# Optimization experiments

Measured on AMD Instinct MI355X. Metric: run time of the kernel, lower is better.

The kernel has to match this reference:

```python
import jax, jax.numpy as jnp
import numpy as np

# dims
N = 50000      # total nodes in merged batch graph
M = 250000     # edges for GNN propagation
E = 200000     # candidate edges scored by mixture-Bernoulli head
MAXN = 512     # max_num_nodes (padded adjacency row length)
H = 128        # hidden_dim = embedding_dim = msg_dim
EF = 128       # edge_feat_dim = 2 * att_edge_dim
ATT = 128      # att_hidden_dim
K = 20         # num_mix_component
L = 3          # num_GNN_layers
S = 512        # num_subgraph
B = 16         # batch of graphs
C = 1          # num_canonical_order


def setup_inputs() -> dict:
    key = jax.random.key(0)
    ks = list(jax.random.split(key, 64))
    it = iter(ks)
    nk = lambda: next(it)
    d = {}
    d['node_feat'] = jax.random.normal(nk(), (N, MAXN), jnp.float32)
    d['edge'] = jax.random.randint(nk(), (M, 2), 0, N, dtype=jnp.int32)
    d['edge_feat'] = jax.random.normal(nk(), (M, EF), jnp.float32)
    d['node_idx_gnn'] = jax.random.randint(nk(), (E, 2), 0, N, dtype=jnp.int32)
    d['label'] = (jax.random.uniform(nk(), (E,)) < 0.1).astype(jnp.float32)
    # even sorted partition of E candidate edges into S subgraphs (all nonempty)
    d['subgraph_idx'] = ((jnp.arange(E) * S) // E).astype(jnp.int32)
    # bc_idx = repeat_interleave(arange(B*C), subgraphs_per_graph)
    d['bc_idx'] = jnp.repeat(jnp.arange(B * C, dtype=jnp.int32), S // (B * C))
    # params
    def lin(k, out_d, in_d):
        return jax.random.normal(k, (out_d, in_d), jnp.float32) * (1.0 / np.sqrt(in_d))
    d['dec_W'] = lin(nk(), H, MAXN); d['dec_b'] = jnp.zeros((H,), jnp.float32)
    d['msg_W1'] = jnp.stack([lin(nk(), H, H + EF) for _ in range(L)])
    d['msg_b1'] = jnp.zeros((L, H), jnp.float32)
    d['msg_W2'] = jnp.stack([lin(nk(), H, H) for _ in range(L)])
    d['msg_b2'] = jnp.zeros((L, H), jnp.float32)
    d['att_W1'] = jnp.stack([lin(nk(), ATT, H + EF) for _ in range(L)])
    d['att_b1'] = jnp.zeros((L, ATT), jnp.float32)
    d['att_W2'] = jnp.stack([lin(nk(), H, ATT) for _ in range(L)])
    d['att_b2'] = jnp.zeros((L, H), jnp.float32)
    d['gru_Wih'] = jnp.stack([lin(nk(), 3 * H, H) for _ in range(L)])
    d['gru_bih'] = jnp.zeros((L, 3 * H), jnp.float32)
    d['gru_Whh'] = jnp.stack([lin(nk(), 3 * H, H) for _ in range(L)])
    d['gru_bhh'] = jnp.zeros((L, 3 * H), jnp.float32)
    d['th_W1'] = lin(nk(), H, H); d['th_b1'] = jnp.zeros((H,), jnp.float32)
    d['th_W2'] = lin(nk(), H, H); d['th_b2'] = jnp.zeros((H,), jnp.float32)
    d['th_W3'] = lin(nk(), K, H); d['th_b3'] = jnp.zeros((K,), jnp.float32)
    d['al_W1'] = lin(nk(), H, H); d['al_b1'] = jnp.zeros((H,), jnp.float32)
    d['al_W2'] = lin(nk(), H, H); d['al_b2'] = jnp.zeros((H,), jnp.float32)
    d['al_W3'] = lin(nk(), K, H); d['al_b3'] = jnp.zeros((K,), jnp.float32)
    return d


def _gran_forward(node_feat, edge_feat, label, dec_W, dec_b, msg_W1, msg_b1,
                  msg_W2, msg_b2, att_W1, att_b1, att_W2, att_b2, gru_Wih,
                  gru_bih, gru_Whh, gru_bhh, th_W1, th_b1, th_W2, th_b2,
                  th_W3, th_b3, al_W1, al_b1, al_W2, al_b2, al_W3, al_b3,
                  edge, node_idx_gnn, subgraph_idx, bc_idx):
    n = node_feat.shape[0]
    # decoder_input: Linear(max_num_nodes -> embedding_dim)
    state = node_feat @ dec_W.T + dec_b  # [N, H]
    src, dst = edge[:, 0], edge[:, 1]
    for l in range(L):
        if l > 0:
            state = jax.nn.relu(state)
        # _prop: gather diff, msg MLP, sigmoid attention gate, scatter-sum, GRU
        diff = state[src] - state[dst]                       # [M, H]
        ei = jnp.concatenate([diff, edge_feat], axis=1)      # [M, H+EF]
        msg = jax.nn.relu(ei @ msg_W1[l].T + msg_b1[l]) @ msg_W2[l].T + msg_b2[l]
        att = jax.nn.sigmoid(jax.nn.relu(ei @ att_W1[l].T + att_b1[l]) @ att_W2[l].T + att_b2[l])
        agg = jax.ops.segment_sum(msg * att, dst, num_segments=n)  # [N, H]
        # torch GRUCell
        gi = agg @ gru_Wih[l].T + gru_bih[l]
        gh = state @ gru_Whh[l].T + gru_bhh[l]
        i_r, i_z, i_n = jnp.split(gi, 3, axis=-1)
        h_r, h_z, h_n = jnp.split(gh, 3, axis=-1)
        r = jax.nn.sigmoid(i_r + h_r)
        z = jax.nn.sigmoid(i_z + h_z)
        nn_ = jnp.tanh(i_n + r * h_n)
        state = (1.0 - z) * nn_ + z * state
    # mixture-Bernoulli heads on candidate-edge node-state diffs
    d2 = state[node_idx_gnn[:, 0]] - state[node_idx_gnn[:, 1]]  # [E, H]
    def mlp3(x, W1, b1, W2, b2, W3, b3):
        h = jax.nn.relu(x @ W1.T + b1)
        h = jax.nn.relu(h @ W2.T + b2)
        return h @ W3.T + b3
    log_theta = mlp3(d2, th_W1, th_b1, th_W2, th_b2, th_W3, th_b3)  # [E, K]
    log_alpha = mlp3(d2, al_W1, al_b1, al_W2, al_b2, al_W3, al_b3)  # [E, K]
    # mixture_bernoulli_loss (pos_weight = 1.0)
    y = label[:, None]
    adj_loss = jax.nn.softplus(-log_theta) + (1.0 - y) * log_theta  # BCEWithLogits, [E, K]
    const = jax.ops.segment_sum(jnp.ones((label.shape[0],), log_theta.dtype), subgraph_idx, num_segments=S)
    reduce_adj = jax.ops.segment_sum(adj_loss, subgraph_idx, num_segments=S)     # [S, K]
    reduce_la = jax.ops.segment_sum(log_alpha, subgraph_idx, num_segments=S)
    reduce_la = jax.nn.log_softmax(reduce_la / const[:, None], axis=-1)
    log_prob = jax.scipy.special.logsumexp(-reduce_adj + reduce_la, axis=1)      # [S]
    bc_log_prob = jax.ops.segment_sum(log_prob, bc_idx, num_segments=B * C)
    bc_const = jax.ops.segment_sum(const, bc_idx, num_segments=B * C)
    bc_loss = (bc_log_prob / bc_const).reshape(B, C)
    b_loss = jax.scipy.special.logsumexp(bc_loss, axis=1)  # logsumexp over orderings
    return jnp.mean(-b_loss)


def reference(node_feat, edge, edge_feat, node_idx_gnn, label, subgraph_idx,
              bc_idx, dec_W, dec_b, msg_W1, msg_b1, msg_W2, msg_b2, att_W1,
              att_b1, att_W2, att_b2, gru_Wih, gru_bih, gru_Whh, gru_bhh,
              th_W1, th_b1, th_W2, th_b2, th_W3, th_b3, al_W1, al_b1, al_W2,
              al_b2, al_W3, al_b3):
    return _gran_forward(node_feat, edge_feat, label, dec_W, dec_b, msg_W1,
                         msg_b1, msg_W2, msg_b2, att_W1, att_b1, att_W2,
                         att_b2, gru_Wih, gru_bih, gru_Whh, gru_bhh, th_W1,
                         th_b1, th_W2, th_b2, th_W3, th_b3, al_W1, al_b1,
                         al_W2, al_b2, al_W3, al_b3, edge, node_idx_gnn,
                         subgraph_idx, bc_idx)
```

## Files before the change

kernel.cpp:

```cpp
#include <hip/hip_runtime.h>
#include <cstdint>
#include <cstddef>


typedef __bf16 bf16x8 __attribute__((ext_vector_type(8)));
typedef short  s16x8  __attribute__((ext_vector_type(8)));
typedef short  s16x4  __attribute__((ext_vector_type(4)));
typedef float  f32x4  __attribute__((ext_vector_type(4)));

__device__ inline unsigned short f2bf(float f) {
    return __builtin_bit_cast(unsigned short, (__bf16)f);
}
__device__ inline float bf2f(unsigned short b) {
    return __uint_as_float(((unsigned int)b) << 16);
}
__device__ inline unsigned int pk2(float a, float b) {
    return ((unsigned int)f2bf(b) << 16) | f2bf(a);
}
__device__ inline f32x4 MFMA(bf16x8 a, bf16x8 b, f32x4 c) {
    return __builtin_amdgcn_mfma_f32_16x16x32_bf16(a, b, c, 0, 0, 0);
}

__device__ inline bf16x8 ld_swz(const char* lds, int row, int unit) {
    return *(const bf16x8*)(lds + row * 256 + ((unit ^ (row & 7)) << 4));
}
__device__ inline void hid_write(char* HID, int h0, int erow, s16x4 s4) {
    int unit = h0 >> 3;
    *(s16x4*)(HID + erow * 256 + ((unit ^ (erow & 7)) << 4) + ((h0 & 4) << 1)) = s4;
}
__device__ inline bf16x8 ldA(const short* __restrict__ Wb, int K, int row, int koff) {
    return *(const bf16x8*)(Wb + (size_t)row * K + koff);
}
__device__ inline bf16x8 ld_f32_frag(const float* __restrict__ p) {
    float4 a = *(const float4*)p, b = *(const float4*)(p + 4);
    s16x8 s;
    s[0] = f2bf(a.x); s[1] = f2bf(a.y); s[2] = f2bf(a.z); s[3] = f2bf(a.w);
    s[4] = f2bf(b.x); s[5] = f2bf(b.y); s[6] = f2bf(b.z); s[7] = f2bf(b.w);
    return __builtin_bit_cast(bf16x8, s);
}

#define NPACK 31
struct PrepackArgs {
    const float* src[NPACK];
    short*       dst[NPACK];
    int stride[NPACK];
    int rows[NPACK];
    int rowsTot[NPACK];
    int cols[NPACK];
};

__global__ void prepack(PrepackArgs a) {
    int e = blockIdx.y;
    int row = blockIdx.x;
    if (row >= a.rowsTot[e]) return;
    int c8 = threadIdx.x;
    if (c8 * 8 >= a.cols[e]) return;
    s16x8 s = {};
    if (row < a.rows[e]) {
        const float* p = a.src[e] + (size_t)row * a.stride[e] + c8 * 8;
        float4 x = *(const float4*)p, y = *(const float4*)(p + 4);
        s[0] = f2bf(x.x); s[1] = f2bf(x.y); s[2] = f2bf(x.z); s[3] = f2bf(x.w);
        s[4] = f2bf(y.x); s[5] = f2bf(y.y); s[6] = f2bf(y.z); s[7] = f2bf(y.w);
    }
    *(s16x8*)(a.dst[e] + (size_t)row * a.cols[e] + c8 * 8) = s;
}

__device__ inline void proj_gemm_store(const char* ST, char* PJ,
                                       const short* __restrict__ projW,
                                       short* __restrict__ proj,
                                       int rb, int R, int tid)
{
    const int l = tid & 63, w = tid >> 6;
    f32x4 accP[2][2][4] = {};
#pragma unroll
    for (int ks = 0; ks < 4; ++ks) {
        int koff = ks * 32 + (l >> 4) * 8;
        bf16x8 aw[2][2];
#pragma unroll
        for (int pc = 0; pc < 2; ++pc)
#pragma unroll
            for (int mt = 0; mt < 2; ++mt)
                aw[pc][mt] = ldA(projW, 128, pc * 128 + 32 * w + 16 * mt + (l & 15), koff);
#pragma unroll
        for (int n = 0; n < 4; ++n) {
            bf16x8 b = ld_swz(ST, 16 * n + (l & 15), ks * 4 + (l >> 4));
#pragma unroll
            for (int pc = 0; pc < 2; ++pc)
#pragma unroll
                for (int mt = 0; mt < 2; ++mt)
                    accP[pc][mt][n] = MFMA(aw[pc][mt], b, accP[pc][mt][n]);
        }
    }
    const int half = w >> 1;
#pragma unroll
    for (int hh = 0; hh < 2; ++hh) {
        __syncthreads();
        if (half == hh) {
#pragma unroll
            for (int pc = 0; pc < 2; ++pc)
#pragma unroll
                for (int mt = 0; mt < 2; ++mt) {
                    int h0 = 32 * w + 16 * mt + ((l >> 4) << 2);
                    int colp = 2 * h0 + 4 * pc - 128 * hh;
#pragma unroll
                    for (int n = 0; n < 4; ++n) {
                        f32x4 v = accP[pc][mt][n];
                        s16x4 s4;
                        s4[0] = f2bf(v[0]); s4[1] = f2bf(v[1]);
                        s4[2] = f2bf(v[2]); s4[3] = f2bf(v[3]);
                        hid_write(PJ, colp, 16 * n + (l & 15), s4);
                    }
                }
        }
        __syncthreads();
#pragma unroll
        for (int p2 = 0; p2 < 4; ++p2) {
            int row = p2 * 16 + (tid >> 4);
            int r = rb + row;
            if (r < R) {
                bf16x8 v = ld_swz(PJ, row, tid & 15);
                *(s16x8*)(proj + (size_t)r * 256 + hh * 128 + (tid & 15) * 8) =
                    __builtin_bit_cast(s16x8, v);
            }
        }
    }
}

__global__ __launch_bounds__(256, 2)
void dec_proj(const float* __restrict__ nf, int R,
              const short* __restrict__ decWb, const float* __restrict__ bias,
              const short* __restrict__ projW,
              short* __restrict__ sOut, short* __restrict__ proj)
{
    __shared__ char ST[16384];
    __shared__ char PJ[16384];
    const int tid = threadIdx.x, l = tid & 63, w = tid >> 6;
    const int rb = blockIdx.x * 64;

    const float* brow[4];
#pragma unroll
    for (int n = 0; n < 4; ++n) {
        int row = rb + 16 * n + (l & 15); if (row >= R) row = R - 1;
        brow[n] = nf + (size_t)row * 512;
    }

    f32x4 acc[2][4] = {};
    for (int kc = 0; kc < 512; kc += 128) {
#pragma unroll
        for (int ks = 0; ks < 4; ++ks) {
            int koff = kc + ks * 32 + (l >> 4) * 8;
            bf16x8 a0 = ldA(decWb, 512, 32 * w + (l & 15), koff);
            bf16x8 a1 = ldA(decWb, 512, 32 * w + 16 + (l & 15), koff);
#pragma unroll
            for (int n = 0; n < 4; ++n) {
                bf16x8 b = ld_f32_frag(brow[n] + koff);
                acc[0][n] = MFMA(a0, b, acc[0][n]);
                acc[1][n] = MFMA(a1, b, acc[1][n]);
            }
        }
    }
#pragma unroll
    for (int mt = 0; mt < 2; ++mt) {
        int c0 = 32 * w + 16 * mt + ((l >> 4) << 2);
        float4 bv = *(const float4*)&bias[c0];
#pragma unroll
        for (int n = 0; n < 4; ++n) {
            f32x4 v = acc[mt][n];
            s16x4 s4;
            s4[0] = f2bf(v[0] + bv.x); s4[1] = f2bf(v[1] + bv.y);
            s4[2] = f2bf(v[2] + bv.z); s4[3] = f2bf(v[3] + bv.w);
            hid_write(ST, c0, 16 * n + (l & 15), s4);
        }
    }
    __syncthreads();
#pragma unroll
    for (int p2 = 0; p2 < 4; ++p2) {
        int row = p2 * 16 + (tid >> 4);
        int r = rb + row;
        if (r < R) {
            bf16x8 v = ld_swz(ST, row, tid & 15);
            *(s16x8*)(sOut + (size_t)r * 128 + (tid & 15) * 8) =
                __builtin_bit_cast(s16x8, v);
        }
    }
    proj_gemm_store(ST, PJ, projW, proj, rb, R, tid);
}

template<int HAS_PROJ>
__global__ __launch_bounds__(256, 2)
void node_fused(const short* __restrict__ aggb, const short* __restrict__ sin_,
                const short* __restrict__ Wih, const short* __restrict__ Whh,
                const float* __restrict__ bih, const float* __restrict__ bhh,
                const short* __restrict__ projW,
                short* __restrict__ sOut, short* __restrict__ proj, int R)
{
    __shared__ char ST[16384];
    __shared__ char PJ[16384];
    const int tid = threadIdx.x, l = tid & 63, w = tid >> 6;
    const int rb = blockIdx.x * 64;

    const short* arow[4];
    const short* srow[4];
#pragma unroll
    for (int n = 0; n < 4; ++n) {
        int row = rb + 16 * n + (l & 15); if (row >= R) row = R - 1;
        arow[n] = aggb + (size_t)row * 128;
        srow[n] = sin_ + (size_t)row * 128;
    }
    s16x4 svv[2][4];
#pragma unroll
    for (int mt = 0; mt < 2; ++mt) {
        int c0 = 32 * w + 16 * mt + ((l >> 4) << 2);
#pragma unroll
        for (int n = 0; n < 4; ++n)
            svv[mt][n] = *(const s16x4*)(srow[n] + c0);
    }

    unsigned int rpk[2][4][2], zpk[2][4][2];

    for (int p = 0; p < 3; ++p) {
        f32x4 gia[2][4] = {}, gha[2][4] = {};
#pragma unroll
        for (int ks = 0; ks < 4; ++ks) {
            int koff = ks * 32 + (l >> 4) * 8;
            bf16x8 ai0 = ldA(Wih, 128, p * 128 + 32 * w + (l & 15), koff);
            bf16x8 ai1 = ldA(Wih, 128, p * 128 + 32 * w + 16 + (l & 15), koff);
            bf16x8 ah0 = ldA(Whh, 128, p * 128 + 32 * w + (l & 15), koff);
            bf16x8 ah1 = ldA(Whh, 128, p * 128 + 32 * w + 16 + (l & 15), koff);
#pragma unroll
            for (int n = 0; n < 4; ++n) {
                bf16x8 ba = *(const bf16x8*)(arow[n] + koff);
                bf16x8 bs = *(const bf16x8*)(srow[n] + koff);
                gia[0][n] = MFMA(ai0, ba, gia[0][n]);
                gia[1][n] = MFMA(ai1, ba, gia[1][n]);
                gha[0][n] = MFMA(ah0, bs, gha[0][n]);
                gha[1][n] = MFMA(ah1, bs, gha[1][n]);
            }
        }
#pragma unroll
        for (int mt = 0; mt < 2; ++mt) {
            int c0 = 32 * w + 16 * mt + ((l >> 4) << 2);
            float4 bi = *(const float4*)&bih[p * 128 + c0];
            float4 bh = *(const float4*)&bhh[p * 128 + c0];
            float biv[4] = {bi.x, bi.y, bi.z, bi.w};
            float bhv[4] = {bh.x, bh.y, bh.z, bh.w};
#pragma unroll
            for (int n = 0; n < 4; ++n) {
                float gv[4], hv[4];
#pragma unroll
                for (int q = 0; q < 4; ++q) {
                    gv[q] = gia[mt][n][q] + biv[q];
                    hv[q] = gha[mt][n][q] + bhv[q];
                }
                if (p == 0) {
                    rpk[mt][n][0] = pk2(1.f / (1.f + expf(-(gv[0] + hv[0]))),
                                        1.f / (1.f + expf(-(gv[1] + hv[1]))));
                    rpk[mt][n][1] = pk2(1.f / (1.f + expf(-(gv[2] + hv[2]))),
                                        1.f / (1.f + expf(-(gv[3] + hv[3]))));
                } else if (p == 1) {
                    zpk[mt][n][0] = pk2(1.f / (1.f + expf(-(gv[0] + hv[0]))),
                                        1.f / (1.f + expf(-(gv[1] + hv[1]))));
                    zpk[mt][n][1] = pk2(1.f / (1.f + expf(-(gv[2] + hv[2]))),
                                        1.f / (1.f + expf(-(gv[3] + hv[3]))));
                } else {
                    s16x4 s4;
#pragma unroll
                    for (int q = 0; q < 4; ++q) {
                        unsigned int ru = rpk[mt][n][q >> 1], zu = zpk[mt][n][q >> 1];
                        float r = bf2f((unsigned short)((q & 1) ? (ru >> 16) : (ru & 0xffffu)));
                        float z = bf2f((unsigned short)((q & 1) ? (zu >> 16) : (zu & 0xffffu)));
                        float nn = tanhf(gv[q] + r * hv[q]);
                        float o = (1.f - z) * nn + z * bf2f((unsigned short)svv[mt][n][q]);
                        s4[q] = f2bf(HAS_PROJ ? fmaxf(o, 0.f) : o);
                    }
                    hid_write(ST, c0, 16 * n + (l & 15), s4);
                }
            }
        }
    }
    __syncthreads();
#pragma unroll
    for (int p2 = 0; p2 < 4; ++p2) {
        int row = p2 * 16 + (tid >> 4);
        int r = rb + row;
        if (r < R) {
            bf16x8 v = ld_swz(ST, row, tid & 15);
            *(s16x8*)(sOut + (size_t)r * 128 + (tid & 15) * 8) =
                __builtin_bit_cast(s16x8, v);
        }
    }
    if (HAS_PROJ)
        proj_gemm_store(ST, PJ, projW, proj, rb, R, tid);
}

__global__ __launch_bounds__(256, 3)
void edge_fused2(const short* __restrict__ efc,
                 const int* __restrict__ srcs, const int* __restrict__ dsts,
                 const short* __restrict__ proj,
                 const short* __restrict__ mW1b, const short* __restrict__ mW2,
                 const short* __restrict__ aW1b, const short* __restrict__ aW2,
                 const float* __restrict__ mb1, const float* __restrict__ mb2,
                 const float* __restrict__ ab1, const float* __restrict__ ab2,
                 short* __restrict__ msgatt, int M, int ntiles)
{
    __shared__ char HIDm[16384];
    __shared__ char HIDa[16384];
    const int tid = threadIdx.x, l = tid & 63, w = tid >> 6;
    int q = ntiles >> 3, r = ntiles & 7;
    int xcd = blockIdx.x & 7, o = blockIdx.x >> 3;
    int tile = (xcd < r ? xcd * (q + 1) : r * (q + 1) + (xcd - r) * q) + o;
    const int pb = tile * 64;

    const char* erow[4];
    s16x8 psv[2][4], pdv[2][4];
    {
#pragma unroll
        for (int n = 0; n < 4; ++n) {
            int pos = pb + 16 * n + (l & 15); if (pos >= M) pos = M - 1;
            int sv = srcs[pos], dv = dsts[pos];
            erow[n] = (const char*)(efc + (size_t)pos * 128);
#pragma unroll
            for (int mt = 0; mt < 2; ++mt) {
                int off = 2 * (32 * w + 16 * mt + ((l >> 4) << 2));
                psv[mt][n] = *(const s16x8*)(proj + (size_t)sv * 256 + off);
                pdv[mt][n] = *(const s16x8*)(proj + (size_t)dv * 256 + off);
            }
        }
    }

    f32x4 accm[2][4] = {}, acca[2][4] = {};
#pragma unroll
    for (int ks = 0; ks < 4; ++ks) {
        int koff = ks * 32 + (l >> 4) * 8;
        bf16x8 am0 = ldA(mW1b, 128, 32 * w + (l & 15), koff);
        bf16x8 am1 = ldA(mW1b, 128, 32 * w + 16 + (l & 15), koff);
        bf16x8 aa0 = ldA(aW1b, 128, 32 * w + (l & 15), koff);
        bf16x8 aa1 = ldA(aW1b, 128, 32 * w + 16 + (l & 15), koff);
#pragma unroll
        for (int n = 0; n < 4; ++n) {
            bf16x8 b = *(const bf16x8*)(erow[n] + koff * 2);
            accm[0][n] = MFMA(am0, b, accm[0][n]);
            accm[1][n] = MFMA(am1, b, accm[1][n]);
            acca[0][n] = MFMA(aa0, b, acca[0][n]);
            acca[1][n] = MFMA(aa1, b, acca[1][n]);
        }
    }
#pragma unroll
    for (int mt = 0; mt < 2; ++mt) {
        int h0 = 32 * w + 16 * mt + ((l >> 4) << 2);
        float4 bm = *(const float4*)&mb1[h0];
        float4 ba = *(const float4*)&ab1[h0];
        float bmv[4] = {bm.x, bm.y, bm.z, bm.w};
        float bav[4] = {ba.x, ba.y, ba.z, ba.w};
#pragma unroll
        for (int n = 0; n < 4; ++n) {
            s16x8 ps = psv[mt][n], pd = pdv[mt][n];
            f32x4 vm = accm[mt][n], va = acca[mt][n];
            s16x4 sm, sa;
#pragma unroll
            for (int qq = 0; qq < 4; ++qq) {
                float m_ = vm[qq] + bmv[qq] + bf2f((unsigned short)ps[qq])
                           - bf2f((unsigned short)pd[qq]);
                float a_ = va[qq] + bav[qq] + bf2f((unsigned short)ps[qq + 4])
                           - bf2f((unsigned short)pd[qq + 4]);
                sm[qq] = f2bf(fmaxf(m_, 0.f));
                sa[qq] = f2bf(fmaxf(a_, 0.f));
            }
            hid_write(HIDm, h0, 16 * n + (l & 15), sm);
            hid_write(HIDa, h0, 16 * n + (l & 15), sa);
        }
    }
    __syncthreads();

    f32x4 acc2m[2][4] = {}, acc2a[2][4] = {};
#pragma unroll
    for (int ks = 0; ks < 4; ++ks) {
        int koff = ks * 32 + (l >> 4) * 8;
        bf16x8 wm0 = ldA(mW2, 128, 32 * w + (l & 15), koff);
        bf16x8 wm1 = ldA(mW2, 128, 32 * w + 16 + (l & 15), koff);
        bf16x8 wa0 = ldA(aW2, 128, 32 * w + (l & 15), koff);
        bf16x8 wa1 = ldA(aW2, 128, 32 * w + 16 + (l & 15), koff);
#pragma unroll
        for (int n = 0; n < 4; ++n) {
            bf16x8 bm = ld_swz(HIDm, 16 * n + (l & 15), ks * 4 + (l >> 4));
            bf16x8 ba = ld_swz(HIDa, 16 * n + (l & 15), ks * 4 + (l >> 4));
            acc2m[0][n] = MFMA(wm0, bm, acc2m[0][n]);
            acc2m[1][n] = MFMA(wm1, bm, acc2m[1][n]);
            acc2a[0][n] = MFMA(wa0, ba, acc2a[0][n]);
            acc2a[1][n] = MFMA(wa1, ba, acc2a[1][n]);
        }
    }
    __syncthreads();
#pragma unroll
    for (int mt = 0; mt < 2; ++mt) {
        int c0 = 32 * w + 16 * mt + ((l >> 4) << 2);
        float4 bm2 = *(const float4*)&mb2[c0];
        float4 ba2 = *(const float4*)&ab2[c0];
#pragma unroll
        for (int n = 0; n < 4; ++n) {
            f32x4 m_ = acc2m[mt][n], a_ = acc2a[mt][n];
            float o0 = (m_[0] + bm2.x) / (1.f + expf(-(a_[0] + ba2.x)));
            float o1 = (m_[1] + bm2.y) / (1.f + expf(-(a_[1] + ba2.y)));
            float o2 = (m_[2] + bm2.z) / (1.f + expf(-(a_[2] + ba2.z)));
            float o3 = (m_[3] + bm2.w) / (1.f + expf(-(a_[3] + ba2.w)));
            s16x4 s4;
            s4[0] = f2bf(o0); s4[1] = f2bf(o1); s4[2] = f2bf(o2); s4[3] = f2bf(o3);
            hid_write(HIDm, c0, 16 * n + (l & 15), s4);
        }
    }
    __syncthreads();
#pragma unroll
    for (int p2 = 0; p2 < 4; ++p2) {
        int row = p2 * 16 + (tid >> 4);
        int pos = pb + row;
        if (pos < M) {
            bf16x8 v = ld_swz(HIDm, row, tid & 15);
            *(s16x8*)(msgatt + (size_t)pos * 128 + (tid & 15) * 8) =
                __builtin_bit_cast(s16x8, v);
        }
    }
}

__global__ __launch_bounds__(256, 4)
void mlp_loss(const short* __restrict__ sP, const int* __restrict__ gidx,
              const float* __restrict__ label, const int* __restrict__ sg,
              const short* __restrict__ thW1, const short* __restrict__ thW2,
              const short* __restrict__ thW3,
              const float* __restrict__ thb1, const float* __restrict__ thb2,
              const float* __restrict__ thb3,
              const short* __restrict__ alW1, const short* __restrict__ alW2,
              const short* __restrict__ alW3,
              const float* __restrict__ alb1, const float* __restrict__ alb2,
              const float* __restrict__ alb3,
              float* __restrict__ radj, float* __restrict__ rla,
              float* __restrict__ cntS, int E, int S)
{
    __shared__ char D2T[16384];
    __shared__ char HID[16384];
    __shared__ float sadj[2][20];
    __shared__ float sla[2][20];
    __shared__ float scnt[2];
    __shared__ int sbase;
    const int tid = threadIdx.x, l = tid & 63, w = tid >> 6;
    const int eb = blockIdx.x * 64;

    if (tid == 0) sbase = sg[eb];
    if (tid < 40) { sadj[tid / 20][tid % 20] = 0.f; sla[tid / 20][tid % 20] = 0.f; }
    if (tid < 2) scnt[tid] = 0.f;

    for (int i = tid; i < 64 * 16; i += 256) {
        int row = i >> 4, u = i & 15;
        int e = eb + row; if (e >= E) e = E - 1;
        int2 ab = *(const int2*)&gidx[2 * (size_t)e];
        s16x8 x = *(const s16x8*)(sP + (size_t)ab.x * 128 + u * 8);
        s16x8 y = *(const s16x8*)(sP + (size_t)ab.y * 128 + u * 8);
        s16x8 d;
#pragma unroll
        for (int j = 0; j < 8; ++j)
            d[j] = f2bf(bf2f((unsigned short)x[j]) - bf2f((unsigned short)y[j]));
        *(s16x8*)(D2T + row * 256 + ((u ^ (row & 7)) << 4)) = d;
    }
    __syncthreads();

    for (int pass = 0; pass < 2; ++pass) {
        const short* W1 = pass ? alW1 : thW1;
        const short* W2 = pass ? alW2 : thW2;
        const short* W3 = pass ? alW3 : thW3;
        const float* b1 = pass ? alb1 : thb1;
        const float* b2 = pass ? alb2 : thb2;
        const float* b3 = pass ? alb3 : thb3;

        f32x4 acc[2][4] = {};
#pragma unroll
        for (int ks = 0; ks < 4; ++ks) {
            int koff = ks * 32 + (l >> 4) * 8;
            bf16x8 a0 = ldA(W1, 128, 32 * w + (l & 15), koff);
            bf16x8 a1 = ldA(W1, 128, 32 * w + 16 + (l & 15), koff);
#pragma unroll
            for (int n = 0; n < 4; ++n) {
                bf16x8 b = ld_swz(D2T, 16 * n + (l & 15), ks * 4 + (l >> 4));
                acc[0][n] = MFMA(a0, b, acc[0][n]);
                acc[1][n] = MFMA(a1, b, acc[1][n]);
            }
        }
        __syncthreads();
#pragma unroll
        for (int mt = 0; mt < 2; ++mt) {
            int h0 = 32 * w + 16 * mt + ((l >> 4) << 2);
            float4 bv = *(const float4*)&b1[h0];
#pragma unroll
            for (int n = 0; n < 4; ++n) {
                f32x4 v = acc[mt][n];
                s16x4 s4;
                s4[0] = f2bf(fmaxf(v[0] + bv.x, 0.f));
                s4[1] = f2bf(fmaxf(v[1] + bv.y, 0.f));
                s4[2] = f2bf(fmaxf(v[2] + bv.z, 0.f));
                s4[3] = f2bf(fmaxf(v[3] + bv.w, 0.f));
                hid_write(HID, h0, 16 * n + (l & 15), s4);
            }
        }
        __syncthreads();
        f32x4 acc2[2][4] = {};
#pragma unroll
        for (int ks = 0; ks < 4; ++ks) {
            int koff = ks * 32 + (l >> 4) * 8;
            bf16x8 a0 = ldA(W2, 128, 32 * w + (l & 15), koff);
            bf16x8 a1 = ldA(W2, 128, 32 * w + 16 + (l & 15), koff);
#pragma unroll
            for (int n = 0; n < 4; ++n) {
                bf16x8 b = ld_swz(HID, 16 * n + (l & 15), ks * 4 + (l >> 4));
                acc2[0][n] = MFMA(a0, b, acc2[0][n]);
                acc2[1][n] = MFMA(a1, b, acc2[1][n]);
            }
        }
        __syncthreads();
#pragma unroll
        for (int mt = 0; mt < 2; ++mt) {
            int h0 = 32 * w + 16 * mt + ((l >> 4) << 2);
            float4 bv = *(const float4*)&b2[h0];
#pragma unroll
            for (int n = 0; n < 4; ++n) {
                f32x4 v = acc2[mt][n];
                s16x4 s4;
                s4[0] = f2bf(fmaxf(v[0] + bv.x, 0.f));
                s4[1] = f2bf(fmaxf(v[1] + bv.y, 0.f));
                s4[2] = f2bf(fmaxf(v[2] + bv.z, 0.f));
                s4[3] = f2bf(fmaxf(v[3] + bv.w, 0.f));
                hid_write(HID, h0, 16 * n + (l & 15), s4);
            }
        }
        __syncthreads();
        f32x4 acc3[2] = {};
#pragma unroll
        for (int ks = 0; ks < 4; ++ks) {
            int koff = ks * 32 + (l >> 4) * 8;
            bf16x8 a0 = ldA(W3, 128, (l & 15), koff);
            bf16x8 a1 = ldA(W3, 128, 16 + (l & 15), koff);
            bf16x8 b = ld_swz(HID, 16 * w + (l & 15), ks * 4 + (l >> 4));
            acc3[0] = MFMA(a0, b, acc3[0]);
            acc3[1] = MFMA(a1, b, acc3[1]);
        }
        {
            int e = eb + 16 * w + (l & 15);
            if (e < E) {
                int ls = sg[e] - sbase;
                if (ls < 0) ls = 0; if (ls > 1) ls = 1;
                float y = (pass == 0) ? label[e] : 0.f;
#pragma unroll
                for (int mt = 0; mt < 2; ++mt) {
                    int c0 = 16 * mt + ((l >> 4) << 2);
                    if (c0 < 20) {
#pragma unroll
                        for (int qq = 0; qq < 4; ++qq) {
                            int k = c0 + qq;
                            if (k < 20) {
                                float t = acc3[mt][qq] + b3[k];
                                if (pass == 0) {
                                    float sp = fmaxf(-t, 0.f) + log1pf(expf(-fabsf(t)));
                                    atomicAdd(&sadj[ls][k], sp + (1.f - y) * t);
                                } else {
                                    atomicAdd(&sla[ls][k], t);
                                }
                            }
                        }
                    }
                }
            }
        }
        __syncthreads();
    }

    if (tid < 64) {
        int e = eb + tid;
        if (e < E) {
            int ls = sg[e] - sbase;
            if (ls >= 0 && ls < 2) atomicAdd(&scnt[ls], 1.f);
        }
    }
    __syncthreads();
    if (tid < 40) {
        int ls = tid / 20, k = tid % 20;
        int s = sbase + ls;
        if (s < S) {
            float v = sadj[ls][k], v2 = sla[ls][k];
            if (v  != 0.f) atomicAdd(&radj[s * 20 + k], v);
            if (v2 != 0.f) atomicAdd(&rla[s * 20 + k], v2);
        }
    }
    if (tid < 2) {
        int s = sbase + tid;
        if (s < S && scnt[tid] != 0.f) atomicAdd(&cntS[s], scnt[tid]);
    }
}

__global__ void csr_count(const int* __restrict__ edge, int* __restrict__ cnt, int M) {
    int e = blockIdx.x * 256 + threadIdx.x;
    if (e < M) atomicAdd(&cnt[edge[2 * (size_t)e + 1]], 1);
}

__global__ void csr_scan(const int* __restrict__ cnt, int* __restrict__ rowptr,
                         int* __restrict__ wofs, int N)
{
    __shared__ int part[1024];
    int t = threadIdx.x;
    int chunk = (N + 1023) / 1024;
    int b0 = t * chunk, b1 = b0 + chunk; if (b1 > N) b1 = N; if (b0 > N) b0 = N;
    int s = 0;
    for (int i = b0; i < b1; ++i) s += cnt[i];
    part[t] = s;
    __syncthreads();
    for (int off = 1; off < 1024; off <<= 1) {
        int v = (t >= off) ? part[t - off] : 0;
        __syncthreads();
        part[t] += v;
        __syncthreads();
    }
    int run = (t ? part[t - 1] : 0);
    for (int i = b0; i < b1; ++i) { rowptr[i] = run; wofs[i] = run; run += cnt[i]; }
    if (t == 1023) rowptr[N] = run;
}

__global__ void csr_scatter2(const int* __restrict__ edge, int* __restrict__ wofs,
                             int* __restrict__ eidx, int* __restrict__ srcs,
                             int* __restrict__ dsts, int M)
{
    int e = blockIdx.x * 256 + threadIdx.x;
    if (e < M) {
        int2 sd = *(const int2*)&edge[2 * (size_t)e];
        int p = atomicAdd(&wofs[sd.y], 1);
        eidx[p] = e; srcs[p] = sd.x; dsts[p] = sd.y;
    }
}

__global__ void ef_gather(const float* __restrict__ ef, const int* __restrict__ eidx,
                          short* __restrict__ efc, int M)
{
    long i = (long)blockIdx.x * 256 + threadIdx.x;
    if (i >= (long)M * 16) return;
    int p = (int)(i >> 4), u = (int)(i & 15);
    int e = eidx[p];
    const float* sp = ef + (size_t)e * 128 + u * 8;
    float4 a = *(const float4*)sp, b = *(const float4*)(sp + 4);
    s16x8 s;
    s[0] = f2bf(a.x); s[1] = f2bf(a.y); s[2] = f2bf(a.z); s[3] = f2bf(a.w);
    s[4] = f2bf(b.x); s[5] = f2bf(b.y); s[6] = f2bf(b.z); s[7] = f2bf(b.w);
    *(s16x8*)(efc + (size_t)p * 128 + u * 8) = s;
}

__global__ __launch_bounds__(256)
void agg_gather3(const short* __restrict__ msgatt, const int* __restrict__ rowptr,
                 short* __restrict__ aggb, int N)
{
    int wid = blockIdx.x * 4 + (threadIdx.x >> 6);
    int l = threadIdx.x & 63;
    int v = wid * 4 + (l >> 4);
    int u = l & 15;
    if (v >= N) return;
    int b = rowptr[v], e = rowptr[v + 1];
    float acc[8] = {};
    for (int i = b; i < e; ++i) {
        s16x8 x = *(const s16x8*)(msgatt + (size_t)i * 128 + u * 8);
#pragma unroll
        for (int j = 0; j < 8; ++j) acc[j] += bf2f((unsigned short)x[j]);
    }
    s16x8 o;
#pragma unroll
    for (int j = 0; j < 8; ++j) o[j] = f2bf(acc[j]);
    *(s16x8*)(aggb + (size_t)v * 128 + u * 8) = o;
}

__global__ void final_kernel(const float* __restrict__ radj, const float* __restrict__ rla,
                             const float* __restrict__ cnt, const int* __restrict__ bc_idx,
                             float* __restrict__ out)
{
    __shared__ float bcl[16], bcc[16];
    const int s = threadIdx.x;
    if (s < 16) { bcl[s] = 0.f; bcc[s] = 0.f; }
    __syncthreads();
    float c = cnt[s];
    float x[20];
    float mx = -1e30f;
#pragma unroll
    for (int k = 0; k < 20; ++k) { x[k] = rla[s * 20 + k] / c; mx = fmaxf(mx, x[k]); }
    float se = 0.f;
#pragma unroll
    for (int k = 0; k < 20; ++k) se += expf(x[k] - mx);
    float lse = mx + logf(se);
    float t[20];
    float m2 = -1e30f;
#pragma unroll
    for (int k = 0; k < 20; ++k) { t[k] = -radj[s * 20 + k] + x[k] - lse; m2 = fmaxf(m2, t[k]); }
    float s2 = 0.f;
#pragma unroll
    for (int k = 0; k < 20; ++k) s2 += expf(t[k] - m2);
    float lp = m2 + logf(s2);
    atomicAdd(&bcl[bc_idx[s]], lp);
    atomicAdd(&bcc[bc_idx[s]], c);
    __syncthreads();
    if (s == 0) {
        float a = 0.f;
        for (int b = 0; b < 16; ++b) a += bcl[b] / bcc[b];
        out[0] = -a / 16.f;
    }
}

extern "C" void kernel_launch(void* const* d_in, const int* in_sizes, int n_in,
                              void* d_out, int out_size, void* d_ws, size_t ws_size,
                              hipStream_t stream)
{
    const float* node_feat = (const float*)d_in[0];
    const int*   edge      = (const int*)  d_in[1];
    const float* edge_feat = (const float*)d_in[2];
    const int*   gnn_idx   = (const int*)  d_in[3];
    const float* label     = (const float*)d_in[4];
    const int*   sg_idx    = (const int*)  d_in[5];
    const int*   bc_idx    = (const int*)  d_in[6];
    const float* dec_W  = (const float*)d_in[7];
    const float* dec_b  = (const float*)d_in[8];
    const float* msg_W1 = (const float*)d_in[9];
    const float* msg_b1 = (const float*)d_in[10];
    const float* msg_W2 = (const float*)d_in[11];
    const float* msg_b2 = (const float*)d_in[12];
    const float* att_W1 = (const float*)d_in[13];
    const float* att_b1 = (const float*)d_in[14];
    const float* att_W2 = (const float*)d_in[15];
    const float* att_b2 = (const float*)d_in[16];
    const float* gru_Wih = (const float*)d_in[17];
    const float* gru_bih = (const float*)d_in[18];
    const float* gru_Whh = (const float*)d_in[19];
    const float* gru_bhh = (const float*)d_in[20];
    const float* th_W1 = (const float*)d_in[21];
    const float* th_b1 = (const float*)d_in[22];
    const float* th_W2 = (const float*)d_in[23];
    const float* th_b2 = (const float*)d_in[24];
    const float* th_W3 = (const float*)d_in[25];
    const float* th_b3 = (const float*)d_in[26];
    const float* al_W1 = (const float*)d_in[27];
    const float* al_b1 = (const float*)d_in[28];
    const float* al_W2 = (const float*)d_in[29];
    const float* al_b2 = (const float*)d_in[30];
    const float* al_W3 = (const float*)d_in[31];
    const float* al_b3 = (const float*)d_in[32];

    const int N = in_sizes[0] / 512;
    const int M = in_sizes[1] / 2;
    const int E = in_sizes[3] / 2;
    const int S = in_sizes[6];

    size_t off = 0;
    auto alloc = [&](size_t bytes) {
        char* p = (char*)d_ws + off;
        off += (bytes + 255) & ~(size_t)255;
        return p;
    };
    short* decWb  = (short*)alloc((size_t)128 * 512 * 2);
    short* projWb = (short*)alloc((size_t)3 * 256 * 128 * 2);
    short* mW1bB  = (short*)alloc((size_t)3 * 128 * 128 * 2);
    short* aW1bB  = (short*)alloc((size_t)3 * 128 * 128 * 2);
    short* mW2B   = (short*)alloc((size_t)3 * 128 * 128 * 2);
    short* aW2B   = (short*)alloc((size_t)3 * 128 * 128 * 2);
    short* gihB   = (short*)alloc((size_t)3 * 384 * 128 * 2);
    short* ghhB   = (short*)alloc((size_t)3 * 384 * 128 * 2);
    short* thW1B  = (short*)alloc((size_t)128 * 128 * 2);
    short* thW2B  = (short*)alloc((size_t)128 * 128 * 2);
    short* thW3B  = (short*)alloc((size_t)32 * 128 * 2);
    short* alW1B  = (short*)alloc((size_t)128 * 128 * 2);
    short* alW2B  = (short*)alloc((size_t)128 * 128 * 2);
    short* alW3B  = (short*)alloc((size_t)32 * 128 * 2);
    short* sA     = (short*)alloc((size_t)N * 128 * 2);
    short* sB     = (short*)alloc((size_t)N * 128 * 2);
    short* sP     = (short*)alloc((size_t)N * 128 * 2);
    short* efc    = (short*)alloc((size_t)M * 128 * 2);
    short* msgatt = (short*)alloc((size_t)M * 128 * 2);
    short* proj   = (short*)alloc((size_t)N * 256 * 2);
    short* aggb   = (short*)alloc((size_t)N * 128 * 2);
    int*   cntN   = (int*)  alloc((size_t)N * 4);
    int*   wofs   = (int*)  alloc((size_t)N * 4);
    int*   rowptr = (int*)  alloc((size_t)(N + 1) * 4);
    int*   eidx   = (int*)  alloc((size_t)M * 4);
    int*   srcs   = (int*)  alloc((size_t)M * 4);
    int*   dsts   = (int*)  alloc((size_t)M * 4);
    float* radj   = (float*)alloc((size_t)S * 20 * 4);
    float* rla    = (float*)alloc((size_t)S * 20 * 4);
    float* cntS   = (float*)alloc((size_t)S * 4);

    PrepackArgs pa;
    int ei = 0;
    auto add = [&](const float* s, short* d, int stride, int rows, int rowsTot, int cols) {
        pa.src[ei] = s; pa.dst[ei] = d; pa.stride[ei] = stride;
        pa.rows[ei] = rows; pa.rowsTot[ei] = rowsTot; pa.cols[ei] = cols; ++ei;
    };
    add(dec_W, decWb, 512, 128, 128, 512);
    for (int l = 0; l < 3; ++l) {
        add(msg_W1 + (size_t)l * 128 * 256,       projWb + (size_t)l * 256 * 128,          256, 128, 128, 128);
        add(att_W1 + (size_t)l * 128 * 256,       projWb + (size_t)l * 256 * 128 + 16384,  256, 128, 128, 128);
        add(msg_W1 + (size_t)l * 128 * 256 + 128, mW1bB + (size_t)l * 16384,               256, 128, 128, 128);
        add(att_W1 + (size_t)l * 128 * 256 + 128, aW1bB + (size_t)l * 16384,               256, 128, 128, 128);
        add(msg_W2 + (size_t)l * 16384,           mW2B + (size_t)l * 16384,                128, 128, 128, 128);
        add(att_W2 + (size_t)l * 16384,           aW2B + (size_t)l * 16384,                128, 128, 128, 128);
        add(gru_Wih + (size_t)l * 49152,          gihB + (size_t)l * 49152,                128, 384, 384, 128);
        add(gru_Whh + (size_t)l * 49152,          ghhB + (size_t)l * 49152,                128, 384, 384, 128);
    }
    add(th_W1, thW1B, 128, 128, 128, 128);
    add(th_W2, thW2B, 128, 128, 128, 128);
    add(th_W3, thW3B, 128, 20, 32, 128);
    add(al_W1, alW1B, 128, 128, 128, 128);
    add(al_W2, alW2B, 128, 128, 128, 128);
    add(al_W3, alW3B, 128, 20, 32, 128);

    const dim3 blk(256);
    const int gN64 = (N + 63) / 64;
    const int gE64 = (E + 63) / 64;
    const int gMt  = (M + 255) / 256;
    const int ntilesM = (M + 63) / 64;
    const int gAgg = (N + 15) / 16;

    hipMemsetAsync(radj, 0, (size_t)(S * 20 * 2 + S) * 4, stream);
    hipMemsetAsync(cntN, 0, (size_t)N * 4, stream);

    prepack<<<dim3(384, NPACK), dim3(64), 0, stream>>>(pa);

    csr_count   <<<gMt, blk, 0, stream>>>(edge, cntN, M);
    csr_scan    <<<1, 1024, 0, stream>>>(cntN, rowptr, wofs, N);
    csr_scatter2<<<gMt, blk, 0, stream>>>(edge, wofs, eidx, srcs, dsts, M);
    ef_gather   <<<(int)(((long)M * 16 + 255) / 256), blk, 0, stream>>>(edge_feat, eidx, efc, M);

    dec_proj<<<gN64, blk, 0, stream>>>(node_feat, N, decWb, dec_b, projWb, sA, proj);

    short* bufs[2] = { sA, sB };
    for (int l = 0; l < 3; ++l) {
        short* sin  = bufs[l & 1];
        short* sout = (l == 2) ? sP : bufs[(l + 1) & 1];
        edge_fused2<<<ntilesM, blk, 0, stream>>>(efc, srcs, dsts, proj,
            mW1bB + (size_t)l * 16384, mW2B + (size_t)l * 16384,
            aW1bB + (size_t)l * 16384, aW2B + (size_t)l * 16384,
            msg_b1 + l * 128, msg_b2 + l * 128,
            att_b1 + l * 128, att_b2 + l * 128,
            msgatt, M, ntilesM);
        agg_gather3<<<gAgg, blk, 0, stream>>>(msgatt, rowptr, aggb, N);
        if (l < 2) {
            node_fused<1><<<gN64, blk, 0, stream>>>(aggb, sin,
                gihB + (size_t)l * 49152, ghhB + (size_t)l * 49152,
                gru_bih + l * 384, gru_bhh + l * 384,
                projWb + (size_t)(l + 1) * 256 * 128, sout, proj, N);
        } else {
            node_fused<0><<<gN64, blk, 0, stream>>>(aggb, sin,
                gihB + (size_t)l * 49152, ghhB + (size_t)l * 49152,
                gru_bih + l * 384, gru_bhh + l * 384,
                nullptr, sout, nullptr, N);
        }
    }

    mlp_loss<<<gE64, blk, 0, stream>>>(sP, gnn_idx, label, sg_idx,
        thW1B, thW2B, thW3B, th_b1, th_b2, th_b3,
        alW1B, alW2B, alW3B, al_b1, al_b2, al_b3,
        radj, rla, cntS, E, S);
    final_kernel<<<1, S, 0, stream>>>(radj, rla, cntS, bc_idx, (float*)d_out);
}
```

Baseline: 1.205 ms.

## Enlarge edge tile to 128 rows, split mlp_loss heads across wave pairs

The edge MLP kernel now runs 512-thread blocks covering 128 edges, with two groups of four waves sharing the same weight rows. Source and destination projection loads move from the prologue to the epilogue to reduce live registers. mlp_loss runs the theta and alpha heads at the same time on separate wave pairs, each with its own LDS buffer. Its per-subgraph reduction now uses ballot counts and wave shuffles in place of many shared atomics. The larger tiles and doubled LDS may lower occupancy, and delaying the gathers exposes their latency later in the kernel.

Measured after the change: 1.340 ms. +11.3%, slower.

```diff
diff --git a/kernel.cpp b/kernel.cpp
--- a/kernel.cpp
+++ b/kernel.cpp
@@ -293,8 +293,8 @@
         proj_gemm_store(ST, PJ, projW, proj, rb, R, tid);
 }
 
-__global__ __launch_bounds__(256, 3)
-void edge_fused2(const short* __restrict__ efc,
+__global__ __launch_bounds__(512, 4)
+void edge_fused3(const short* __restrict__ efc,
                  const int* __restrict__ srcs, const int* __restrict__ dsts,
                  const short* __restrict__ proj,
                  const short* __restrict__ mW1b, const short* __restrict__ mW2,
@@ -303,39 +303,32 @@
                  const float* __restrict__ ab1, const float* __restrict__ ab2,
                  short* __restrict__ msgatt, int M, int ntiles)
 {
-    __shared__ char HIDm[16384];
-    __shared__ char HIDa[16384];
+    __shared__ char HIDm[32768];
+    __shared__ char HIDa[32768];
     const int tid = threadIdx.x, l = tid & 63, w = tid >> 6;
+    const int wq = w >> 2, wh = w & 3;
     int q = ntiles >> 3, r = ntiles & 7;
     int xcd = blockIdx.x & 7, o = blockIdx.x >> 3;
     int tile = (xcd < r ? xcd * (q + 1) : r * (q + 1) + (xcd - r) * q) + o;
-    const int pb = tile * 64;
-
+    const int pb = tile * 128;
+
+    int srcv[4], dstv[4];
     const char* erow[4];
-    s16x8 psv[2][4], pdv[2][4];
-    {
-#pragma unroll
-        for (int n = 0; n < 4; ++n) {
-            int pos = pb + 16 * n + (l & 15); if (pos >= M) pos = M - 1;
-            int sv = srcs[pos], dv = dsts[pos];
-            erow[n] = (const char*)(efc + (size_t)pos * 128);
-#pragma unroll
-            for (int mt = 0; mt < 2; ++mt) {
-                int off = 2 * (32 * w + 16 * mt + ((l >> 4) << 2));
-                psv[mt][n] = *(const s16x8*)(proj + (size_t)sv * 256 + off);
-                pdv[mt][n] = *(const s16x8*)(proj + (size_t)dv * 256 + off);
-            }
-        }
+#pragma unroll
+    for (int n = 0; n < 4; ++n) {
+        int pos = pb + 64 * wq + 16 * n + (l & 15); if (pos >= M) pos = M - 1;
+        srcv[n] = srcs[pos]; dstv[n] = dsts[pos];
+        erow[n] = (const char*)(efc + (size_t)pos * 128);
     }
 
     f32x4 accm[2][4] = {}, acca[2][4] = {};
 #pragma unroll
     for (int ks = 0; ks < 4; ++ks) {
         int koff = ks * 32 + (l >> 4) * 8;
-        bf16x8 am0 = ldA(mW1b, 128, 32 * w + (l & 15), koff);
-        bf16x8 am1 = ldA(mW1b, 128, 32 * w + 16 + (l & 15), koff);
-        bf16x8 aa0 = ldA(aW1b, 128, 32 * w + (l & 15), koff);
-        bf16x8 aa1 = ldA(aW1b, 128, 32 * w + 16 + (l & 15), koff);
+        bf16x8 am0 = ldA(mW1b, 128, 32 * wh + (l & 15), koff);
+        bf16x8 am1 = ldA(mW1b, 128, 32 * wh + 16 + (l & 15), koff);
+        bf16x8 aa0 = ldA(aW1b, 128, 32 * wh + (l & 15), koff);
+        bf16x8 aa1 = ldA(aW1b, 128, 32 * wh + 16 + (l & 15), koff);
 #pragma unroll
         for (int n = 0; n < 4; ++n) {
             bf16x8 b = *(const bf16x8*)(erow[n] + koff * 2);
@@ -347,14 +340,15 @@
     }
 #pragma unroll
     for (int mt = 0; mt < 2; ++mt) {
-        int h0 = 32 * w + 16 * mt + ((l >> 4) << 2);
+        int h0 = 32 * wh + 16 * mt + ((l >> 4) << 2);
         float4 bm = *(const float4*)&mb1[h0];
         float4 ba = *(const float4*)&ab1[h0];
         float bmv[4] = {bm.x, bm.y, bm.z, bm.w};
         float bav[4] = {ba.x, ba.y, ba.z, ba.w};
 #pragma unroll
         for (int n = 0; n < 4; ++n) {
-            s16x8 ps = psv[mt][n], pd = pdv[mt][n];
+            s16x8 ps = *(const s16x8*)(proj + (size_t)srcv[n] * 256 + 2 * h0);
+            s16x8 pd = *(const s16x8*)(proj + (size_t)dstv[n] * 256 + 2 * h0);
             f32x4 vm = accm[mt][n], va = acca[mt][n];
             s16x4 sm, sa;
 #pragma unroll
@@ -366,8 +360,9 @@
                 sm[qq] = f2bf(fmaxf(m_, 0.f));
                 sa[qq] = f2bf(fmaxf(a_, 0.f));
             }
-            hid_write(HIDm, h0, 16 * n + (l & 15), sm);
-            hid_write(HIDa, h0, 16 * n + (l & 15), sa);
+            int erl = 64 * wq + 16 * n + (l & 15);
+            hid_write(HIDm, h0, erl, sm);
+            hid_write(HIDa, h0, erl, sa);
         }
     }
     __syncthreads();
@@ -376,14 +371,15 @@
 #pragma unroll
     for (int ks = 0; ks < 4; ++ks) {
         int koff = ks * 32 + (l >> 4) * 8;
-        bf16x8 wm0 = ldA(mW2, 128, 32 * w + (l & 15), koff);
-        bf16x8 wm1 = ldA(mW2, 128, 32 * w + 16 + (l & 15), koff);
-        bf16x8 wa0 = ldA(aW2, 128, 32 * w + (l & 15), koff);
-        bf16x8 wa1 = ldA(aW2, 128, 32 * w + 16 + (l & 15), koff);
+        bf16x8 wm0 = ldA(mW2, 128, 32 * wh + (l & 15), koff);
+        bf16x8 wm1 = ldA(mW2, 128, 32 * wh + 16 + (l & 15), koff);
+        bf16x8 wa0 = ldA(aW2, 128, 32 * wh + (l & 15), koff);
+        bf16x8 wa1 = ldA(aW2, 128, 32 * wh + 16 + (l & 15), koff);
 #pragma unroll
         for (int n = 0; n < 4; ++n) {
-            bf16x8 bm = ld_swz(HIDm, 16 * n + (l & 15), ks * 4 + (l >> 4));
-            bf16x8 ba = ld_swz(HIDa, 16 * n + (l & 15), ks * 4 + (l >> 4));
+            int erl = 64 * wq + 16 * n + (l & 15);
+            bf16x8 bm = ld_swz(HIDm, erl, ks * 4 + (l >> 4));
+            bf16x8 ba = ld_swz(HIDa, erl, ks * 4 + (l >> 4));
             acc2m[0][n] = MFMA(wm0, bm, acc2m[0][n]);
             acc2m[1][n] = MFMA(wm1, bm, acc2m[1][n]);
             acc2a[0][n] = MFMA(wa0, ba, acc2a[0][n]);
@@ -393,7 +389,7 @@
     __syncthreads();
 #pragma unroll
     for (int mt = 0; mt < 2; ++mt) {
-        int c0 = 32 * w + 16 * mt + ((l >> 4) << 2);
+        int c0 = 32 * wh + 16 * mt + ((l >> 4) << 2);
         float4 bm2 = *(const float4*)&mb2[c0];
         float4 ba2 = *(const float4*)&ab2[c0];
 #pragma unroll
@@ -405,13 +401,13 @@
             float o3 = (m_[3] + bm2.w) / (1.f + expf(-(a_[3] + ba2.w)));
             s16x4 s4;
             s4[0] = f2bf(o0); s4[1] = f2bf(o1); s4[2] = f2bf(o2); s4[3] = f2bf(o3);
-            hid_write(HIDm, c0, 16 * n + (l & 15), s4);
+            hid_write(HIDm, c0, 64 * wq + 16 * n + (l & 15), s4);
         }
     }
     __syncthreads();
 #pragma unroll
     for (int p2 = 0; p2 < 4; ++p2) {
-        int row = p2 * 16 + (tid >> 4);
+        int row = p2 * 32 + (tid >> 4);
         int pos = pb + row;
         if (pos < M) {
             bf16x8 v = ld_swz(HIDm, row, tid & 15);
@@ -421,7 +417,7 @@
     }
 }
 
-__global__ __launch_bounds__(256, 4)
+__global__ __launch_bounds__(256, 3)
 void mlp_loss(const short* __restrict__ sP, const int* __restrict__ gidx,
               const float* __restrict__ label, const int* __restrict__ sg,
               const short* __restrict__ thW1, const short* __restrict__ thW2,
@@ -436,17 +432,25 @@
               float* __restrict__ cntS, int E, int S)
 {
     __shared__ char D2T[16384];
-    __shared__ char HID[16384];
-    __shared__ float sadj[2][20];
-    __shared__ float sla[2][20];
+    __shared__ char HD[2][16384];
+    __shared__ float sacc[2][2][20];
     __shared__ float scnt[2];
     __shared__ int sbase;
     const int tid = threadIdx.x, l = tid & 63, w = tid >> 6;
+    const int p = w >> 1, wp = w & 1;
     const int eb = blockIdx.x * 64;
 
     if (tid == 0) sbase = sg[eb];
-    if (tid < 40) { sadj[tid / 20][tid % 20] = 0.f; sla[tid / 20][tid % 20] = 0.f; }
-    if (tid < 2) scnt[tid] = 0.f;
+    if (tid < 80) sacc[tid / 40][(tid / 20) & 1][tid % 20] = 0.f;
+
+    if (w == 0) {
+        int e = eb + l;
+        bool valid = e < E;
+        int lsv = valid ? sg[e] - sg[eb] : -1;
+        unsigned long long m0 = __ballot(lsv == 0);
+        unsigned long long m1 = __ballot(lsv == 1);
+        if (l == 0) { scnt[0] = (float)__popcll(m0); scnt[1] = (float)__popcll(m1); }
+    }
 
     for (int i = tid; i < 64 * 16; i += 256) {
         int row = i >> 4, u = i & 15;
@@ -462,31 +466,34 @@
     }
     __syncthreads();
 
-    for (int pass = 0; pass < 2; ++pass) {
-        const short* W1 = pass ? alW1 : thW1;
-        const short* W2 = pass ? alW2 : thW2;
-        const short* W3 = pass ? alW3 : thW3;
-        const float* b1 = pass ? alb1 : thb1;
-        const float* b2 = pass ? alb2 : thb2;
-        const float* b3 = pass ? alb3 : thb3;
-
-        f32x4 acc[2][4] = {};
+    const short* W1 = p ? alW1 : thW1;
+    const short* W2 = p ? alW2 : thW2;
+    const short* W3 = p ? alW3 : thW3;
+    const float* b1 = p ? alb1 : thb1;
+    const float* b2 = p ? alb2 : thb2;
+    const float* b3 = p ? alb3 : thb3;
+    char* HID = HD[p];
+
+    {
+        f32x4 acc[4][4] = {};
 #pragma unroll
         for (int ks = 0; ks < 4; ++ks) {
             int koff = ks * 32 + (l >> 4) * 8;
-            bf16x8 a0 = ldA(W1, 128, 32 * w + (l & 15), koff);
-            bf16x8 a1 = ldA(W1, 128, 32 * w + 16 + (l & 15), koff);
+            bf16x8 a[4];
+#pragma unroll
+            for (int mt = 0; mt < 4; ++mt)
+                a[mt] = ldA(W1, 128, 64 * wp + 16 * mt + (l & 15), koff);
 #pragma unroll
             for (int n = 0; n < 4; ++n) {
                 bf16x8 b = ld_swz(D2T, 16 * n + (l & 15), ks * 4 + (l >> 4));
-                acc[0][n] = MFMA(a0, b, acc[0][n]);
-                acc[1][n] = MFMA(a1, b, acc[1][n]);
+#pragma unroll
+                for (int mt = 0; mt < 4; ++mt)
+                    acc[mt][n] = MFMA(a[mt], b, acc[mt][n]);
             }
         }
-        __syncthreads();
-#pragma unroll
-        for (int mt = 0; mt < 2; ++mt) {
-            int h0 = 32 * w + 16 * mt + ((l >> 4) << 2);
+#pragma unroll
+        for (int mt = 0; mt < 4; ++mt) {
+            int h0 = 64 * wp + 16 * mt + ((l >> 4) << 2);
             float4 bv = *(const float4*)&b1[h0];
 #pragma unroll
             for (int n = 0; n < 4; ++n) {
@@ -499,82 +506,95 @@
                 hid_write(HID, h0, 16 * n + (l & 15), s4);
             }
         }
-        __syncthreads();
-        f32x4 acc2[2][4] = {};
-#pragma unroll
-        for (int ks = 0; ks < 4; ++ks) {
-            int koff = ks * 32 + (l >> 4) * 8;
-            bf16x8 a0 = ldA(W2, 128, 32 * w + (l & 15), koff);
-            bf16x8 a1 = ldA(W2, 128, 32 * w + 16 + (l & 15), koff);
-#pragma unroll
-            for (int n = 0; n < 4; ++n) {
-                bf16x8 b = ld_swz(HID, 16 * n + (l & 15), ks * 4 + (l >> 4));
-                acc2[0][n] = MFMA(a0, b, acc2[0][n]);
-                acc2[1][n] = MFMA(a1, b, acc2[1][n]);
-            }
-        }
-        __syncthreads();
+    }
+    __syncthreads();
+    f32x4 acc2[4][4] = {};
+#pragma unroll
+    for (int ks = 0; ks < 4; ++ks) {
+        int koff = ks * 32 + (l >> 4) * 8;
+        bf16x8 a[4];
+#pragma unroll
+        for (int mt = 0; mt < 4; ++mt)
+            a[mt] = ldA(W2, 128, 64 * wp + 16 * mt + (l & 15), koff);
+#pragma unroll
+        for (int n = 0; n < 4; ++n) {
+            bf16x8 b = ld_swz(HID, 16 * n + (l & 15), ks * 4 + (l >> 4));
+#pragma unroll
+            for (int mt = 0; mt < 4; ++mt)
+                acc2[mt][n] = MFMA(a[mt], b, acc2[mt][n]);
+        }
+    }
+    __syncthreads();
+#pragma unroll
+    for (int mt = 0; mt < 4; ++mt) {
+        int h0 = 64 * wp + 16 * mt + ((l >> 4) << 2);
+        float4 bv = *(const float4*)&b2[h0];
+#pragma unroll
+        for (int n = 0; n < 4; ++n) {
+            f32x4 v = acc2[mt][n];
+            s16x4 s4;
+            s4[0] = f2bf(fmaxf(v[0] + bv.x, 0.f));
+            s4[1] = f2bf(fmaxf(v[1] + bv.y, 0.f));
+            s4[2] = f2bf(fmaxf(v[2] + bv.z, 0.f));
+            s4[3] = f2bf(fmaxf(v[3] + bv.w, 0.f));
+            hid_write(HID, h0, 16 * n + (l & 15), s4);
+        }
+    }
+    __syncthreads();
+    f32x4 acc3[2][2] = {};
+#pragma unroll
+    for (int ks = 0; ks < 4; ++ks) {
+        int koff = ks * 32 + (l >> 4) * 8;
+        bf16x8 a0 = ldA(W3, 128, (l & 15), koff);
+        bf16x8 a1 = ldA(W3, 128, 16 + (l & 15), koff);
+#pragma unroll
+        for (int j = 0; j < 2; ++j) {
+            bf16x8 b = ld_swz(HID, 16 * (2 * wp + j) + (l & 15), ks * 4 + (l >> 4));
+            acc3[0][j] = MFMA(a0, b, acc3[0][j]);
+            acc3[1][j] = MFMA(a1, b, acc3[1][j]);
+        }
+    }
+    {
+        int ej[2]; bool val[2]; float lsf[2], yv[2];
+#pragma unroll
+        for (int j = 0; j < 2; ++j) {
+            ej[j] = eb + 16 * (2 * wp + j) + (l & 15);
+            val[j] = ej[j] < E;
+            lsf[j] = val[j] ? (float)(sg[ej[j]] - sbase) : 0.f;
+            yv[j] = (p == 0 && val[j]) ? label[ej[j]] : 0.f;
+        }
 #pragma unroll
         for (int mt = 0; mt < 2; ++mt) {
-            int h0 = 32 * w + 16 * mt + ((l >> 4) << 2);
-            float4 bv = *(const float4*)&b2[h0];
-#pragma unroll
-            for (int n = 0; n < 4; ++n) {
-                f32x4 v = acc2[mt][n];
-                s16x4 s4;
-                s4[0] = f2bf(fmaxf(v[0] + bv.x, 0.f));
-                s4[1] = f2bf(fmaxf(v[1] + bv.y, 0.f));
-                s4[2] = f2bf(fmaxf(v[2] + bv.z, 0.f));
-                s4[3] = f2bf(fmaxf(v[3] + bv.w, 0.f));
-                hid_write(HID, h0, 16 * n + (l & 15), s4);
-            }
-        }
-        __syncthreads();
-        f32x4 acc3[2] = {};
-#pragma unroll
-        for (int ks = 0; ks < 4; ++ks) {
-            int koff = ks * 32 + (l >> 4) * 8;
-            bf16x8 a0 = ldA(W3, 128, (l & 15), koff);
-            bf16x8 a1 = ldA(W3, 128, 16 + (l & 15), koff);
-            bf16x8 b = ld_swz(HID, 16 * w + (l & 15), ks * 4 + (l >> 4));
-            acc3[0] = MFMA(a0, b, acc3[0]);
-            acc3[1] = MFMA(a1, b, acc3[1]);
-        }
-        {
-            int e = eb + 16 * w + (l & 15);
-            if (e < E) {
-                int ls = sg[e] - sbase;
-                if (ls < 0) ls = 0; if (ls > 1) ls = 1;
-                float y = (pass == 0) ? label[e] : 0.f;
-#pragma unroll
-                for (int mt = 0; mt < 2; ++mt) {
-                    int c0 = 16 * mt + ((l >> 4) << 2);
-                    if (c0 < 20) {
-#pragma unroll
-                        for (int qq = 0; qq < 4; ++qq) {
-                            int k = c0 + qq;
-                            if (k < 20) {
-                                float t = acc3[mt][qq] + b3[k];
-                                if (pass == 0) {
-                                    float sp = fmaxf(-t, 0.f) + log1pf(expf(-fabsf(t)));
-                                    atomicAdd(&sadj[ls][k], sp + (1.f - y) * t);
-                                } else {
-                                    atomicAdd(&sla[ls][k], t);
-                                }
-                            }
+#pragma unroll
+            for (int qq = 0; qq < 4; ++qq) {
+                int k = 16 * mt + ((l >> 4) << 2) + qq;
+                bool kok = k < 20;
+                float bk = kok ? b3[k] : 0.f;
+                float vA = 0.f, vB = 0.f;
+#pragma unroll
+                for (int j = 0; j < 2; ++j) {
+                    if (val[j] && kok) {
+                        float t = acc3[mt][j][qq] + bk;
+                        float v;
+                        if (p == 0) {
+                            float sp = fmaxf(-t, 0.f) + log1pf(expf(-fabsf(t)));
+                            v = sp + (1.f - yv[j]) * t;
+                        } else {
+                            v = t;
                         }
+                        vA += v * (1.f - lsf[j]);
+                        vB += v * lsf[j];
                     }
                 }
+                vA += __shfl_xor(vA, 1); vB += __shfl_xor(vB, 1);
+                vA += __shfl_xor(vA, 2); vB += __shfl_xor(vB, 2);
+                vA += __shfl_xor(vA, 4); vB += __shfl_xor(vB, 4);
+                vA += __shfl_xor(vA, 8); vB += __shfl_xor(vB, 8);
+                if ((l & 15) == 0 && kok) {
+                    atomicAdd(&sacc[p][0][k], vA);
+                    if (vB != 0.f) atomicAdd(&sacc[p][1][k], vB);
+                }
             }
-        }
-        __syncthreads();
-    }
-
-    if (tid < 64) {
-        int e = eb + tid;
-        if (e < E) {
-            int ls = sg[e] - sbase;
-            if (ls >= 0 && ls < 2) atomicAdd(&scnt[ls], 1.f);
         }
     }
     __syncthreads();
@@ -582,7 +602,8 @@
         int ls = tid / 20, k = tid % 20;
         int s = sbase + ls;
         if (s < S) {
-            float v = sadj[ls][k], v2 = sla[ls][k];
+            float v  = sacc[0][ls][k];
+            float v2 = sacc[1][ls][k];
             if (v  != 0.f) atomicAdd(&radj[s * 20 + k], v);
             if (v2 != 0.f) atomicAdd(&rla[s * 20 + k], v2);
         }
@@ -812,7 +833,7 @@
     const int gN64 = (N + 63) / 64;
     const int gE64 = (E + 63) / 64;
     const int gMt  = (M + 255) / 256;
-    const int ntilesM = (M + 63) / 64;
+    const int ntilesM = (M + 127) / 128;
     const int gAgg = (N + 15) / 16;
 
     hipMemsetAsync(radj, 0, (size_t)(S * 20 * 2 + S) * 4, stream);
@@ -831,7 +852,7 @@
     for (int l = 0; l < 3; ++l) {
         short* sin  = bufs[l & 1];
         short* sout = (l == 2) ? sP : bufs[(l + 1) & 1];
-        edge_fused2<<<ntilesM, blk, 0, stream>>>(efc, srcs, dsts, proj,
+        edge_fused3<<<ntilesM, dim3(512), 0, stream>>>(efc, srcs, dsts, proj,
             mW1bB + (size_t)l * 16384, mW2B + (size_t)l * 16384,
             aW1bB + (size_t)l * 16384, aW2B + (size_t)l * 16384,
             msg_b1 + l * 128, msg_b2 + l * 128,
```
